# Optimization experiments

Hardware: AMD Instinct MI355X
Metric: run time of the kernel (lower is better)

## Reference

```python
import jax, jax.numpy as jnp
import numpy as np

DIM = 8          # per-head dim
ATT_EPS = 1e-15
BN_EPS = 1e-6


def setup_inputs() -> dict:
    key = jax.random.key(0)
    ks = jax.random.split(key, 6)
    B, C, H, W = 8, 256, 64, 64
    td = 256                      # heads * dim = 32 * 8
    return {
        'x':      jax.random.normal(ks[0], (B, C, H, W), jnp.float32),
        'w_qkv':  jax.random.normal(ks[1], (3 * td, C), jnp.float32) * 0.05,
        'w_dw':   jax.random.normal(ks[2], (3 * td, 1, 5, 5), jnp.float32) * 0.05,
        'w_pw':   jax.random.normal(ks[3], (96, 8, 8), jnp.float32) * 0.05,   # (groups, out/g, in/g)
        'w_proj': jax.random.normal(ks[4], (C, 2 * td), jnp.float32) * 0.05,
        'bn_gamma': jnp.ones((C,), jnp.float32),
        'bn_beta':  jnp.zeros((C,), jnp.float32),
        'bn_mean':  jnp.zeros((C,), jnp.float32),
        'bn_var':   jnp.ones((C,), jnp.float32),
    }


def _relu_linear_att(ms, H, W):
    # ms: [B, C, H, W] with C = heads * 3*DIM
    B = ms.shape[0]
    d = DIM
    qkv = ms.reshape(B, -1, 3 * d, H * W).transpose(0, 1, 3, 2)   # [B, h, N, 3d]
    q = jax.nn.relu(qkv[..., :d])
    k = jax.nn.relu(qkv[..., d:2 * d])
    v = qkv[..., 2 * d:]
    v = jnp.pad(v, ((0, 0), (0, 0), (0, 0), (0, 1)), constant_values=1.0)  # ones column
    kv = jnp.einsum('bhnd,bhne->bhde', k, v)                       # [B, h, d, d+1]
    out = jnp.einsum('bhnd,bhde->bhne', q, kv)                     # [B, h, N, d+1]
    out = out[..., :-1] / (out[..., -1:] + ATT_EPS)
    return out.transpose(0, 1, 3, 2).reshape(B, -1, H, W)          # [B, h*d, H, W]


def reference(x, w_qkv, w_dw, w_pw, w_proj, bn_gamma, bn_beta, bn_mean, bn_var):
    B, C, H, W = x.shape
    # 1x1 qkv projection
    qkv = jnp.einsum('oc,bchw->bohw', w_qkv, x)                    # [B, 768, H, W]
    # multiscale aggregation: 5x5 depthwise then grouped 1x1 (groups = 3*heads = 96)
    dw = jax.lax.conv_general_dilated(
        qkv, w_dw, window_strides=(1, 1), padding=[(2, 2), (2, 2)],
        dimension_numbers=('NCHW', 'OIHW', 'NCHW'),
        feature_group_count=qkv.shape[1])
    G, O, I = w_pw.shape
    agg = jnp.einsum('goi,bgihw->bgohw', w_pw,
                     dw.reshape(B, G, I, H, W)).reshape(B, G * O, H, W)
    ms = jnp.concatenate([qkv, agg], axis=1)                       # [B, 1536, H, W]
    att = _relu_linear_att(ms, H, W)                               # [B, 512, H, W]
    # proj: 1x1 conv + BatchNorm (eval mode) + identity activation
    p = jnp.einsum('oc,bchw->bohw', w_proj, att)                   # [B, 256, H, W]
    inv = bn_gamma / jnp.sqrt(bn_var + BN_EPS)
    p = p * inv[None, :, None, None] + (bn_beta - bn_mean * inv)[None, :, None, None]
    return x + p
```

## Files before the change

### kernel.cpp

```cpp
#include <hip/hip_runtime.h>
#include <hip/hip_bf16.h>


#define HW 4096
#define ATT_EPS 1e-15f
#define BN_EPS 1e-6f

typedef __attribute__((ext_vector_type(8))) short short8;
typedef __attribute__((ext_vector_type(4))) short short4v;
typedef __attribute__((ext_vector_type(4))) float f32x4;
typedef __attribute__((ext_vector_type(8))) unsigned short u16x8;
typedef __attribute__((ext_vector_type(4))) unsigned short u16x4;

static __device__ inline short f2bf(float f) {
    union { float f; unsigned u; } v; v.f = f;
    unsigned r = v.u + 0x7fff + ((v.u >> 16) & 1);
    return (short)(r >> 16);
}
static __device__ inline float bf2f(unsigned short u) {
    union { unsigned u; float f; } v; v.u = (unsigned)u << 16; return v.f;
}

__global__ __launch_bounds__(256) void prep_w(const float* __restrict__ wproj,
                                              unsigned short* __restrict__ wbf) {
    const int i = (blockIdx.x * 256 + threadIdx.x) * 4;
    float4 v = *(const float4*)&wproj[i];
    u16x4 r = {(unsigned short)f2bf(v.x), (unsigned short)f2bf(v.y),
               (unsigned short)f2bf(v.z), (unsigned short)f2bf(v.w)};
    *(u16x4*)&wbf[i] = r;
}

__global__ __launch_bounds__(256) void qkv_gemm(const float* __restrict__ x,
                                                const float* __restrict__ w,
                                                unsigned short* __restrict__ qkv) {
    __shared__ short A_l[128 * 40];
    __shared__ short B_l[128 * 40];
    const int t  = threadIdx.x;
    const int b  = blockIdx.z;
    const int ob = blockIdx.y * 128;
    const int nb = blockIdx.x * 128;
    const float* xb = x + (size_t)b * 256 * HW;

    const int lane = t & 63, wave = t >> 6;
    const int wo = (wave >> 1) * 64, wn = (wave & 1) * 64;

    f32x4 acc[4][4];
#pragma unroll
    for (int s = 0; s < 4; s++)
#pragma unroll
        for (int u = 0; u < 4; u++) acc[s][u] = (f32x4){0.f, 0.f, 0.f, 0.f};

    const int col4 = (t & 7) * 4;
    const int r0   = t >> 3;
    for (int kb = 0; kb < 256; kb += 32) {
        __syncthreads();
#pragma unroll
        for (int i = 0; i < 4; i++) {
            const int r = r0 + 32 * i;
            float4 v = *(const float4*)&w[(ob + r) * 256 + kb + col4];
            short4v s4 = {f2bf(v.x), f2bf(v.y), f2bf(v.z), f2bf(v.w)};
            *(short4v*)&A_l[r * 40 + col4] = s4;
        }
#pragma unroll
        for (int i = 0; i < 4; i++) {
            const int n4 = (t & 7) + 8 * i;
            float4 v = *(const float4*)&xb[(size_t)(kb + r0) * HW + nb + n4 * 4];
            B_l[(n4 * 4 + 0) * 40 + r0] = f2bf(v.x);
            B_l[(n4 * 4 + 1) * 40 + r0] = f2bf(v.y);
            B_l[(n4 * 4 + 2) * 40 + r0] = f2bf(v.z);
            B_l[(n4 * 4 + 3) * 40 + r0] = f2bf(v.w);
        }
        __syncthreads();

        short8 af[4], bf[4];
#pragma unroll
        for (int s = 0; s < 4; s++)
            af[s] = *(const short8*)&A_l[(wo + s * 16 + (lane & 15)) * 40 + (lane >> 4) * 8];
#pragma unroll
        for (int u = 0; u < 4; u++)
            bf[u] = *(const short8*)&B_l[(wn + u * 16 + (lane & 15)) * 40 + (lane >> 4) * 8];
#pragma unroll
        for (int s = 0; s < 4; s++)
#pragma unroll
            for (int u = 0; u < 4; u++)
                acc[s][u] = __builtin_amdgcn_mfma_f32_16x16x32_bf16(af[s], bf[u], acc[s][u], 0, 0, 0);
    }

#pragma unroll
    for (int s = 0; s < 4; s++)
#pragma unroll
        for (int u = 0; u < 4; u++)
#pragma unroll
            for (int r = 0; r < 4; r++) {
                const int o = ob + wo + s * 16 + (lane >> 4) * 4 + r;
                const int n = nb + wn + u * 16 + (lane & 15);
                qkv[((size_t)b * 768 + o) * HW + n] = (unsigned short)f2bf(acc[s][u][r]);
            }
}

__global__ __launch_bounds__(256, 5) void dw_agg(const unsigned short* __restrict__ qkv,
                                                 const float* __restrict__ wdw,
                                                 const float* __restrict__ wpw,
                                                 unsigned short* __restrict__ agg) {
    __shared__ unsigned short tile_raw[8 + 8 * 20 * 64 + 8];
    __shared__ float wk[8][25];
    __shared__ float pw[64];
    unsigned short* base = tile_raw + 8;
    const int b = blockIdx.z, g = blockIdx.y;
    const int y0 = blockIdx.x * 16;
    const int t = threadIdx.x;

    if (t < 200) wk[t / 25][t % 25] = wdw[(g * 8) * 25 + t];
    if (t < 64)  pw[t] = wpw[g * 64 + t];

#pragma unroll
    for (int k = 0; k < 5; k++) {
        const int i = t + 256 * k;
        const int c8 = i & 7, rr = (i >> 3) % 20, ch = i / 160;
        const int y = y0 - 2 + rr;
        u16x8 v = {0, 0, 0, 0, 0, 0, 0, 0};
        if (y >= 0 && y < 64)
            v = *(const u16x8*)&qkv[((size_t)(b * 768 + g * 8 + ch)) * HW + y * 64 + c8 * 8];
        *(u16x8*)&base[i * 8] = v;
    }
    __syncthreads();

    const int tx = t & 15, ty = t >> 4;
    float out[8][4];
#pragma unroll
    for (int o = 0; o < 8; o++)
#pragma unroll
        for (int j = 0; j < 4; j++) out[o][j] = 0.f;

#pragma unroll 1
    for (int ch = 0; ch < 8; ch++) {
        float a0 = 0.f, a1 = 0.f, a2 = 0.f, a3 = 0.f;
#pragma unroll
        for (int dy = 0; dy < 5; dy++) {
            const int off = ch * 1280 + (ty + dy) * 64 + tx * 4;
            u16x4 L  = *(const u16x4*)&base[off - 4];
            u16x4 C  = *(const u16x4*)&base[off];
            u16x4 R  = *(const u16x4*)&base[off + 4];
            float win[8];
            win[0] = (tx == 0)  ? 0.f : bf2f(L[2]);
            win[1] = (tx == 0)  ? 0.f : bf2f(L[3]);
            win[2] = bf2f(C[0]); win[3] = bf2f(C[1]);
            win[4] = bf2f(C[2]); win[5] = bf2f(C[3]);
            win[6] = (tx == 15) ? 0.f : bf2f(R[0]);
            win[7] = (tx == 15) ? 0.f : bf2f(R[1]);
#pragma unroll
            for (int dx = 0; dx < 5; dx++) {
                const float wv = wk[ch][dy * 5 + dx];
                a0 += wv * win[dx + 0];
                a1 += wv * win[dx + 1];
                a2 += wv * win[dx + 2];
                a3 += wv * win[dx + 3];
            }
        }
#pragma unroll
        for (int o = 0; o < 8; o++) {
            const float wv = pw[o * 8 + ch];
            out[o][0] += wv * a0; out[o][1] += wv * a1;
            out[o][2] += wv * a2; out[o][3] += wv * a3;
        }
    }

#pragma unroll
    for (int o = 0; o < 8; o++) {
        u16x4 rv = {(unsigned short)f2bf(out[o][0]), (unsigned short)f2bf(out[o][1]),
                    (unsigned short)f2bf(out[o][2]), (unsigned short)f2bf(out[o][3])};
        *(u16x4*)&agg[((size_t)(b * 768 + g * 8 + o)) * HW + (y0 + ty) * 64 + tx * 4] = rv;
    }
}

__global__ __launch_bounds__(256) void kv_pass(const unsigned short* __restrict__ qkv,
                                               const unsigned short* __restrict__ agg,
                                               float* __restrict__ kvout) {
    const int h = blockIdx.x, b = blockIdx.y;
    const unsigned short* buf = (h < 32) ? qkv : agg;
    const int cbase = (h < 32) ? h * 24 : (h - 32) * 24;
    const u16x4* kp4 = (const u16x4*)(buf + ((size_t)b * 768 + cbase + 8)  * HW);
    const u16x4* vp4 = (const u16x4*)(buf + ((size_t)b * 768 + cbase + 16) * HW);

    float acc[8][9];
#pragma unroll
    for (int d = 0; d < 8; d++)
#pragma unroll
        for (int e = 0; e < 9; e++) acc[d][e] = 0.f;

#pragma unroll
    for (int k = 0; k < 4; k++) {
        const int nn = threadIdx.x + k * 256;
        float kk[8][4];
#pragma unroll
        for (int d = 0; d < 8; d++) {
            u16x4 v = kp4[d * 1024 + nn];
            kk[d][0] = fmaxf(bf2f(v.x), 0.f); kk[d][1] = fmaxf(bf2f(v.y), 0.f);
            kk[d][2] = fmaxf(bf2f(v.z), 0.f); kk[d][3] = fmaxf(bf2f(v.w), 0.f);
        }
#pragma unroll
        for (int e = 0; e < 8; e++) {
            u16x4 vr = vp4[e * 1024 + nn];
            float v0 = bf2f(vr.x), v1 = bf2f(vr.y), v2 = bf2f(vr.z), v3 = bf2f(vr.w);
#pragma unroll
            for (int d = 0; d < 8; d++)
                acc[d][e] += kk[d][0] * v0 + kk[d][1] * v1 + kk[d][2] * v2 + kk[d][3] * v3;
        }
#pragma unroll
        for (int d = 0; d < 8; d++)
            acc[d][8] += kk[d][0] + kk[d][1] + kk[d][2] + kk[d][3];
    }

    __shared__ float red[4][72];
    const int lane = threadIdx.x & 63, wv = threadIdx.x >> 6;
#pragma unroll
    for (int d = 0; d < 8; d++) {
#pragma unroll
        for (int e = 0; e < 9; e++) {
            float v = acc[d][e];
            v += __shfl_xor(v, 1);  v += __shfl_xor(v, 2);
            v += __shfl_xor(v, 4);  v += __shfl_xor(v, 8);
            v += __shfl_xor(v, 16); v += __shfl_xor(v, 32);
            if (lane == 0) red[wv][d * 9 + e] = v;
        }
    }
    __syncthreads();
    if (threadIdx.x < 72) {
        float s = red[0][threadIdx.x] + red[1][threadIdx.x] +
                  red[2][threadIdx.x] + red[3][threadIdx.x];
        kvout[((size_t)(b * 64 + h)) * 72 + threadIdx.x] = s;
    }
}

__global__ __launch_bounds__(256) void att_pass(const unsigned short* __restrict__ qkv,
                                                const unsigned short* __restrict__ agg,
                                                const float* __restrict__ kvbuf,
                                                unsigned short* __restrict__ att_f) {
    __shared__ float kvl[72];
    const int h = blockIdx.y, b = blockIdx.z;
    const int t = threadIdx.x;
    if (t < 72) kvl[t] = kvbuf[((size_t)(b * 64 + h)) * 72 + t];
    __syncthreads();

    const unsigned short* buf = (h < 32) ? qkv : agg;
    const int cbase = (h & 31) * 24;
    const int n0 = (blockIdx.x * 256 + t) * 8;
    const unsigned short* qp = buf + ((size_t)b * 768 + cbase) * HW + n0;

    float q[8][8];
#pragma unroll
    for (int d = 0; d < 8; d++) {
        u16x8 v = *(const u16x8*)&qp[(size_t)d * HW];
#pragma unroll
        for (int j = 0; j < 8; j++) q[d][j] = fmaxf(bf2f(v[j]), 0.f);
    }

    unsigned short* op = att_f + (((size_t)(b * 64 + h)) * HW + n0) * 8;
#pragma unroll
    for (int j = 0; j < 8; j++) {
        float num[9];
#pragma unroll
        for (int e = 0; e < 9; e++) num[e] = 0.f;
#pragma unroll
        for (int d = 0; d < 8; d++) {
            const float qv = q[d][j];
            const float* kvh = &kvl[d * 9];
#pragma unroll
            for (int e = 0; e < 9; e++) num[e] += qv * kvh[e];
        }
        const float rden = 1.f / (num[8] + ATT_EPS);
        u16x8 r;
#pragma unroll
        for (int e = 0; e < 8; e++) r[e] = (unsigned short)f2bf(num[e] * rden);
        *(u16x8*)&op[j * 8] = r;
    }
}

__global__ __launch_bounds__(256) void proj_gemm(const unsigned short* __restrict__ wbf,
                                                 const unsigned short* __restrict__ att_f,
                                                 const float* __restrict__ gamma,
                                                 const float* __restrict__ beta,
                                                 const float* __restrict__ mean,
                                                 const float* __restrict__ var,
                                                 const float* __restrict__ x,
                                                 float* __restrict__ out) {
    const int t  = threadIdx.x;
    const int b  = blockIdx.z;
    const int ob = blockIdx.y * 128;
    const int nb = blockIdx.x * 128;
    const int lane = t & 63, wave = t >> 6;
    const int wo = (wave >> 1) * 64, wn = (wave & 1) * 64;

    const int am = lane & 15, ak = lane >> 4;
    const unsigned short* ap0 = wbf + (size_t)(ob + wo + am) * 512 + ak * 8;
    const unsigned short* bp0 = att_f +
        (((size_t)b * 64 + ak) * HW + nb + wn + am) * 8;

    f32x4 acc[4][4];
#pragma unroll
    for (int s = 0; s < 4; s++)
#pragma unroll
        for (int u = 0; u < 4; u++) acc[s][u] = (f32x4){0.f, 0.f, 0.f, 0.f};

    for (int kb = 0; kb < 512; kb += 32) {
        short8 af[4], bf[4];
#pragma unroll
        for (int s = 0; s < 4; s++)
            af[s] = *(const short8*)(ap0 + (size_t)s * 16 * 512 + kb);
#pragma unroll
        for (int u = 0; u < 4; u++)
            bf[u] = *(const short8*)(bp0 + ((size_t)(kb >> 3) * HW + u * 16) * 8);
#pragma unroll
        for (int s = 0; s < 4; s++)
#pragma unroll
            for (int u = 0; u < 4; u++)
                acc[s][u] = __builtin_amdgcn_mfma_f32_16x16x32_bf16(af[s], bf[u], acc[s][u], 0, 0, 0);
    }

#pragma unroll
    for (int s = 0; s < 4; s++) {
        const int o_base = ob + wo + s * 16 + (lane >> 4) * 4;
#pragma unroll
        for (int r = 0; r < 4; r++) {
            const int o = o_base + r;
            const float inv = gamma[o] * rsqrtf(var[o] + BN_EPS);
            const float sh  = beta[o] - mean[o] * inv;
#pragma unroll
            for (int u = 0; u < 4; u++) {
                const int n = nb + wn + u * 16 + (lane & 15);
                const size_t idx = ((size_t)b * 256 + o) * HW + n;
                out[idx] = x[idx] + acc[s][u][r] * inv + sh;
            }
        }
    }
}

extern "C" void kernel_launch(void* const* d_in, const int* in_sizes, int n_in,
                              void* d_out, int out_size, void* d_ws, size_t ws_size,
                              hipStream_t stream) {
    const float* x      = (const float*)d_in[0];
    const float* w_qkv  = (const float*)d_in[1];
    const float* w_dw   = (const float*)d_in[2];
    const float* w_pw   = (const float*)d_in[3];
    const float* w_proj = (const float*)d_in[4];
    const float* gamma  = (const float*)d_in[5];
    const float* beta   = (const float*)d_in[6];
    const float* mean   = (const float*)d_in[7];
    const float* var    = (const float*)d_in[8];
    float* out = (float*)d_out;

    unsigned short* qkv  = (unsigned short*)d_ws;
    unsigned short* agg  = qkv + (size_t)25165824;
    unsigned short* attf = agg + (size_t)25165824;
    unsigned short* wbf  = attf + (size_t)16777216;
    float* kvb = (float*)(wbf + (size_t)131072);

    prep_w  <<<dim3(128),       256, 0, stream>>>(w_proj, wbf);
    qkv_gemm<<<dim3(32, 6, 8),  256, 0, stream>>>(x, w_qkv, qkv);
    dw_agg  <<<dim3(4, 96, 8),  256, 0, stream>>>(qkv, w_dw, w_pw, agg);
    kv_pass <<<dim3(64, 8),     256, 0, stream>>>(qkv, agg, kvb);
    att_pass<<<dim3(2, 64, 8),  256, 0, stream>>>(qkv, agg, kvb, attf);
    proj_gemm<<<dim3(32, 2, 8), 256, 0, stream>>>(wbf, attf,
                                                  gamma, beta, mean, var, x, out);
}
```

Baseline: 253.8 us.

## Compute two output rows per thread in depthwise conv to reuse loaded windows

The depthwise 5x5 plus grouped 1x1 kernel now produces 32 rows per block, with each thread computing two adjacent output rows. Each loaded row window feeds both rows' accumulators, so per-output LDS reads drop and the halo overhead per block shrinks. The cost is a larger shared tile, higher register use (occupancy hint lowered from 5 to 4), and half as many blocks in the grid.

```diff
diff --git a/kernel.cpp b/kernel.cpp
--- a/kernel.cpp
+++ b/kernel.cpp
@@ -98,25 +98,25 @@
             }
 }
 
-__global__ __launch_bounds__(256, 5) void dw_agg(const unsigned short* __restrict__ qkv,
+__global__ __launch_bounds__(256, 4) void dw_agg(const unsigned short* __restrict__ qkv,
                                                  const float* __restrict__ wdw,
                                                  const float* __restrict__ wpw,
                                                  unsigned short* __restrict__ agg) {
-    __shared__ unsigned short tile_raw[8 + 8 * 20 * 64 + 8];
+    __shared__ unsigned short tile_raw[8 + 8 * 36 * 64 + 8];
     __shared__ float wk[8][25];
     __shared__ float pw[64];
     unsigned short* base = tile_raw + 8;
     const int b = blockIdx.z, g = blockIdx.y;
-    const int y0 = blockIdx.x * 16;
+    const int y0 = blockIdx.x * 32;
     const int t = threadIdx.x;
 
     if (t < 200) wk[t / 25][t % 25] = wdw[(g * 8) * 25 + t];
     if (t < 64)  pw[t] = wpw[g * 64 + t];
 
 #pragma unroll
-    for (int k = 0; k < 5; k++) {
+    for (int k = 0; k < 9; k++) {
         const int i = t + 256 * k;
-        const int c8 = i & 7, rr = (i >> 3) % 20, ch = i / 160;
+        const int c8 = i & 7, rr = (i >> 3) % 36, ch = i / 288;
         const int y = y0 - 2 + rr;
         u16x8 v = {0, 0, 0, 0, 0, 0, 0, 0};
         if (y >= 0 && y < 64)
@@ -126,18 +126,25 @@
     __syncthreads();
 
     const int tx = t & 15, ty = t >> 4;
-    float out[8][4];
-#pragma unroll
-    for (int o = 0; o < 8; o++)
-#pragma unroll
-        for (int j = 0; j < 4; j++) out[o][j] = 0.f;
+    float out[2][8][4];
+#pragma unroll
+    for (int oo = 0; oo < 2; oo++)
+#pragma unroll
+        for (int o = 0; o < 8; o++)
+#pragma unroll
+            for (int j = 0; j < 4; j++) out[oo][o][j] = 0.f;
 
 #pragma unroll 1
     for (int ch = 0; ch < 8; ch++) {
-        float a0 = 0.f, a1 = 0.f, a2 = 0.f, a3 = 0.f;
-#pragma unroll
-        for (int dy = 0; dy < 5; dy++) {
-            const int off = ch * 1280 + (ty + dy) * 64 + tx * 4;
+        float a[2][4];
+#pragma unroll
+        for (int oo = 0; oo < 2; oo++)
+#pragma unroll
+            for (int j = 0; j < 4; j++) a[oo][j] = 0.f;
+
+#pragma unroll
+        for (int rr = 0; rr < 6; rr++) {
+            const int off = ch * 2304 + (2 * ty + rr) * 64 + tx * 4;
             u16x4 L  = *(const u16x4*)&base[off - 4];
             u16x4 C  = *(const u16x4*)&base[off];
             u16x4 R  = *(const u16x4*)&base[off + 4];
@@ -148,28 +155,51 @@
             win[4] = bf2f(C[2]); win[5] = bf2f(C[3]);
             win[6] = (tx == 15) ? 0.f : bf2f(R[0]);
             win[7] = (tx == 15) ? 0.f : bf2f(R[1]);
-#pragma unroll
-            for (int dx = 0; dx < 5; dx++) {
-                const float wv = wk[ch][dy * 5 + dx];
-                a0 += wv * win[dx + 0];
-                a1 += wv * win[dx + 1];
-                a2 += wv * win[dx + 2];
-                a3 += wv * win[dx + 3];
+            if (rr < 5) {
+                const float* wr = &wk[ch][rr * 5];
+#pragma unroll
+                for (int dx = 0; dx < 5; dx++) {
+                    const float wv = wr[dx];
+                    a[0][0] += wv * win[dx + 0];
+                    a[0][1] += wv * win[dx + 1];
+                    a[0][2] += wv * win[dx + 2];
+                    a[0][3] += wv * win[dx + 3];
+                }
+            }
+            if (rr >= 1) {
+                const float* wr = &wk[ch][(rr - 1) * 5];
+#pragma unroll
+                for (int dx = 0; dx < 5; dx++) {
+                    const float wv = wr[dx];
+                    a[1][0] += wv * win[dx + 0];
+                    a[1][1] += wv * win[dx + 1];
+                    a[1][2] += wv * win[dx + 2];
+                    a[1][3] += wv * win[dx + 3];
+                }
             }
         }
 #pragma unroll
         for (int o = 0; o < 8; o++) {
             const float wv = pw[o * 8 + ch];
-            out[o][0] += wv * a0; out[o][1] += wv * a1;
-            out[o][2] += wv * a2; out[o][3] += wv * a3;
-        }
-    }
-
-#pragma unroll
-    for (int o = 0; o < 8; o++) {
-        u16x4 rv = {(unsigned short)f2bf(out[o][0]), (unsigned short)f2bf(out[o][1]),
-                    (unsigned short)f2bf(out[o][2]), (unsigned short)f2bf(out[o][3])};
-        *(u16x4*)&agg[((size_t)(b * 768 + g * 8 + o)) * HW + (y0 + ty) * 64 + tx * 4] = rv;
+#pragma unroll
+            for (int oo = 0; oo < 2; oo++) {
+                out[oo][o][0] += wv * a[oo][0];
+                out[oo][o][1] += wv * a[oo][1];
+                out[oo][o][2] += wv * a[oo][2];
+                out[oo][o][3] += wv * a[oo][3];
+            }
+        }
+    }
+
+#pragma unroll
+    for (int oo = 0; oo < 2; oo++) {
+        const int y = y0 + 2 * ty + oo;
+#pragma unroll
+        for (int o = 0; o < 8; o++) {
+            u16x4 rv = {(unsigned short)f2bf(out[oo][o][0]), (unsigned short)f2bf(out[oo][o][1]),
+                        (unsigned short)f2bf(out[oo][o][2]), (unsigned short)f2bf(out[oo][o][3])};
+            *(u16x4*)&agg[((size_t)(b * 768 + g * 8 + o)) * HW + y * 64 + tx * 4] = rv;
+        }
     }
 }
 
@@ -357,7 +387,7 @@
 
     prep_w  <<<dim3(128),       256, 0, stream>>>(w_proj, wbf);
     qkv_gemm<<<dim3(32, 6, 8),  256, 0, stream>>>(x, w_qkv, qkv);
-    dw_agg  <<<dim3(4, 96, 8),  256, 0, stream>>>(qkv, w_dw, w_pw, agg);
+    dw_agg  <<<dim3(2, 96, 8),  256, 0, stream>>>(qkv, w_dw, w_pw, agg);
     kv_pass <<<dim3(64, 8),     256, 0, stream>>>(qkv, agg, kvb);
     att_pass<<<dim3(2, 64, 8),  256, 0, stream>>>(qkv, agg, kvb, attf);
     proj_gemm<<<dim3(32, 2, 8), 256, 0, stream>>>(wbf, attf,
```

Measured after the change: 282.5 us. 1.11x slower.
